# Kernel tuning notes

Hardware: AMD Instinct MI355X
Metric: run time of the kernel (lower is better)

## Reference

```python
import jax, jax.numpy as jnp
import numpy as np

B, T, D = 2, 2048, 2048
H, HD = 8, 128
C = H * HD  # 1024 channels
BT = 64     # chunk size
EPS_RMS = 1.1920929e-07  # torch fp32 finfo eps (RMSNorm default)


def causal_dw_conv(x, w, b):
    # x: [B,T,C], w: [C,4], b: [C]. Equals torch Conv1d(groups=C, k=4, padding=3)[..., :T]
    Bx, Tx, Cx = x.shape
    xp = jnp.pad(x, ((0, 0), (3, 0), (0, 0)))
    out = sum(xp[:, j:j + Tx, :] * w[None, None, :, j] for j in range(4))
    return out + b


def chunk_kda(q, k, v, g):
    # q,k,g: [B,H,T,K]; v: [B,H,T,V]
    Bx, Hx, Tx, K = q.shape
    V = v.shape[-1]
    NT = Tx // BT
    resh = lambda a: a.reshape(Bx, Hx, NT, BT, a.shape[-1])
    q, k, v, g = map(resh, (q, k, v, g))
    gc = jnp.cumsum(g, axis=-2)                        # [B,H,NT,BT,K]
    diff = gc[..., :, None, :] - gc[..., None, :, :]   # [B,H,NT,BT,BT,K]
    tri_incl = jnp.tril(jnp.ones((BT, BT), bool))
    tri_strict = jnp.tril(jnp.ones((BT, BT), bool), -1)
    Aqk = jnp.einsum('bhnik,bhnjk,bhnijk->bhnij', q, k, jnp.exp(diff)) * tri_incl
    Akk = jnp.einsum('bhnik,bhnjk,bhnijk->bhnij', k, k, jnp.exp(-diff)) * tri_strict
    # UT transform: the in-place forward substitution in the source computes
    # A = (I + strictly_lower(Akk))^{-1}; apply it via a unit-lower triangular solve.
    M = Akk + jnp.eye(BT, dtype=q.dtype)
    rhs = jnp.concatenate([jnp.exp(gc) * k, v], axis=-1)
    sol = jax.scipy.linalg.solve_triangular(M, rhs, lower=True, unit_diagonal=True)
    w_, u = sol[..., :K], sol[..., K:]                 # w = A@(exp(gc)*k), u = A@v
    qg = q * jnp.exp(gc)

    def step(S, xs):
        qg_i, k_i, u_i, gc_i, w_i, Aqk_i = xs
        o_i = qg_i @ S + Aqk_i @ (u_i - w_i @ S)
        g_last = gc_i[:, :, -1]                        # [B,H,K]
        decay = jnp.exp(g_last[:, :, None, :] - gc_i)  # [B,H,BT,K]
        S = S * jnp.exp(g_last)[..., :, None] + jnp.einsum('bhck,bhcv->bhkv', k_i * decay, u_i)
        return S, o_i

    xs = tuple(jnp.moveaxis(a, 2, 0) for a in (qg, k, u, gc, w_, Aqk))
    S0 = jnp.zeros((Bx, Hx, K, V), q.dtype)
    S, o = jax.lax.scan(step, S0, xs)
    o = jnp.moveaxis(o, 0, 2).reshape(Bx, Hx, Tx, V)
    return o, S


def _forward(x, Wq, Wk, Wv, conv_q_w, conv_q_b, conv_k_w, conv_k_b, conv_v_w, conv_v_b,
             Wad, Wau, Wb, Wgd, Wgu, norm_w, Wo):
    Bx, Tx, Dx = x.shape
    heads = lambda y: y.reshape(Bx, Tx, H, HD).transpose(0, 2, 1, 3)
    q = heads(causal_dw_conv(x @ Wq, conv_q_w, conv_q_b))
    k = heads(causal_dw_conv(x @ Wk, conv_k_w, conv_k_b))
    q = q / jnp.maximum(jnp.linalg.norm(q, axis=-1, keepdims=True), 1e-12)
    k = k / jnp.maximum(jnp.linalg.norm(k, axis=-1, keepdims=True), 1e-12)
    v = heads(jax.nn.silu(causal_dw_conv(x @ Wv, conv_v_w, conv_v_b)))
    alpha = jax.nn.sigmoid(heads(x @ Wad @ Wau))
    g = jnp.log(jnp.clip(alpha, 1e-6, None))
    _beta = jax.nn.sigmoid(x @ Wb)  # computed in source but unused by chunk_kda
    o, S = chunk_kda(q, k, v, g)
    o = o.transpose(0, 2, 1, 3)                        # [B,T,H,HD]
    o = o * jax.lax.rsqrt(jnp.mean(o * o, axis=-1, keepdims=True) + EPS_RMS) * norm_w
    gate = jax.nn.sigmoid(x @ Wgd @ Wgu).reshape(Bx, Tx, H, HD)
    o = (o * gate).reshape(Bx, Tx, H * HD)
    return o @ Wo, S


def setup_inputs():
    key = jax.random.key(0)
    ks = jax.random.split(key, 16)
    n = lambda k, shape, s=0.02: jax.random.normal(k, shape, jnp.float32) * s
    return {
        'x': jax.random.normal(ks[0], (B, T, D), jnp.float32),
        'Wq': n(ks[1], (D, C)), 'Wk': n(ks[2], (D, C)), 'Wv': n(ks[3], (D, C)),
        'conv_q_w': n(ks[4], (C, 4), 0.1), 'conv_q_b': jnp.zeros((C,), jnp.float32),
        'conv_k_w': n(ks[5], (C, 4), 0.1), 'conv_k_b': jnp.zeros((C,), jnp.float32),
        'conv_v_w': n(ks[6], (C, 4), 0.1), 'conv_v_b': jnp.zeros((C,), jnp.float32),
        'Wad': n(ks[7], (D, HD)), 'Wau': n(ks[8], (HD, C)),
        'Wb': n(ks[9], (D, H)),
        'Wgd': n(ks[10], (D, HD)), 'Wgu': n(ks[11], (HD, C)),
        'norm_w': jnp.ones((HD,), jnp.float32),
        'Wo': n(ks[12], (C, D)),
    }


def reference(x, Wq, Wk, Wv, conv_q_w, conv_q_b, conv_k_w, conv_k_b, conv_v_w, conv_v_b,
              Wad, Wau, Wb, Wgd, Wgu, norm_w, Wo):
    return _forward(x, Wq, Wk, Wv, conv_q_w, conv_q_b, conv_k_w, conv_k_b, conv_v_w, conv_v_b,
                    Wad, Wau, Wb, Wgd, Wgu, norm_w, Wo)
```

## Files before the change

kernel.cpp:

```cpp
#include <hip/hip_runtime.h>
#include <hip/hip_bf16.h>
#include <cstdint>
#include <cstddef>

constexpr int B_  = 2;
constexpr int T_  = 2048;
constexpr int D_  = 2048;
constexpr int H_  = 8;
constexpr int HD_ = 128;
constexpr int C_  = 1024;
constexpr int BT_ = 64;
constexpr int NT_ = 32;
constexpr int M_  = 4096;
constexpr float EPS_RMS = 1.1920929e-07f;

typedef __bf16 bf16x8 __attribute__((ext_vector_type(8)));
typedef float f32x4 __attribute__((ext_vector_type(4)));

typedef const __attribute__((address_space(1))) unsigned int* gptr_t;
typedef __attribute__((address_space(3))) unsigned int* lptr_t;

__device__ __forceinline__ void gload16(const void* g, void* l) {
  __builtin_amdgcn_global_load_lds((gptr_t)g, (lptr_t)l, 16, 0, 0);
}


#define LD_A(base, mq, dst) do { \
    _Pragma("unroll") for (int i_ = 0; i_ < 4; ++i_) \
      _Pragma("unroll") for (int k_ = 0; k_ < 2; ++k_) \
        dst[i_][k_] = *(const bf16x8*)((base) + (mq) * 8192 + i_ * 2048 + k_ * 1024); \
  } while (0)

#define LD_B(base, nq, dst) do { \
    _Pragma("unroll") for (int j_ = 0; j_ < 2; ++j_) \
      _Pragma("unroll") for (int k_ = 0; k_ < 2; ++k_) \
        dst[j_][k_] = *(const bf16x8*)((base) + (nq) * 4096 + j_ * 2048 + k_ * 1024); \
  } while (0)

#define MM_Q(afr, bfr, mq, nq) do { \
    _Pragma("unroll") for (int i_ = 0; i_ < 4; ++i_) \
      _Pragma("unroll") for (int j_ = 0; j_ < 2; ++j_) \
        _Pragma("unroll") for (int k_ = 0; k_ < 2; ++k_) \
          acc[(mq) * 4 + i_][(nq) * 2 + j_] = __builtin_amdgcn_mfma_f32_16x16x32_bf16( \
              afr[i_][k_], bfr[j_][k_], acc[(mq) * 4 + i_][(nq) * 2 + j_], 0, 0, 0); \
  } while (0)

#define STAGE(src, grow0, kc, loff) do { \
    gload16((src) + (size_t)((grow0) + sr0) * 2048 + (kc) + sc0, smem + (loff) + tid * 16); \
    gload16((src) + (size_t)((grow0) + sr1) * 2048 + (kc) + sc1, smem + (loff) + 8192 + tid * 16); \
  } while (0)

#define PH_SYNC_PRE do { \
    __builtin_amdgcn_s_barrier(); \
    asm volatile("s_waitcnt lgkmcnt(0)" ::: "memory"); \
    __builtin_amdgcn_sched_barrier(0); \
    __builtin_amdgcn_s_setprio(1); \
  } while (0)

#define PH_SYNC_POST do { \
    __builtin_amdgcn_s_setprio(0); \
    __builtin_amdgcn_sched_barrier(0); \
    __builtin_amdgcn_s_barrier(); \
  } while (0)

#define PH_SYNC_POST_VM4 do { \
    __builtin_amdgcn_s_setprio(0); \
    __builtin_amdgcn_sched_barrier(0); \
    asm volatile("s_waitcnt vmcnt(4)" ::: "memory"); \
    __builtin_amdgcn_s_barrier(); \
  } while (0)

#define PH_SYNC_POST_VM0 do { \
    __builtin_amdgcn_s_setprio(0); \
    __builtin_amdgcn_sched_barrier(0); \
    asm volatile("s_waitcnt vmcnt(0)" ::: "memory"); \
    __builtin_amdgcn_s_barrier(); \
  } while (0)

__global__ __launch_bounds__(512, 1) void gemm8p(
    const __hip_bfloat16* __restrict__ A_, const __hip_bfloat16* __restrict__ B_,
    __hip_bfloat16* __restrict__ pre, __hip_bfloat16* __restrict__ adb,
    __hip_bfloat16* __restrict__ gdb) {
  __shared__ alignas(16) char smem[131072];
  const int tid = threadIdx.x, lane = tid & 63;
  const int wid = tid >> 6;
  const int wm = (wid >> 2) * 128, wn = (wid & 3) * 64;
  const int lr = lane & 15, lg = lane >> 4;

  const int bid = blockIdx.x;
  const int swz = (bid & 7) * 26 + (bid >> 3);
  const int mt = swz / 13, nt = swz % 13;
  const int m0 = mt * 256, n0g = nt * 256;

  int ob0 = tid * 16;         ob0 ^= ((ob0 >> 9) & 1) << 5;
  int ob1 = (tid + 512) * 16; ob1 ^= ((ob1 >> 9) & 1) << 5;
  const int sr0 = ((ob0 >> 11) << 4) + ((ob0 >> 6) & 15);
  const int sc0 = ((ob0 >> 10) & 1) * 32 + ((ob0 & 63) >> 1);
  const int sr1 = ((ob1 >> 11) << 4) + ((ob1 >> 6) & 15);
  const int sc1 = ((ob1 >> 10) & 1) * 32 + ((ob1 & 63) >> 1);

  const int foff = lr * 64 + ((lg * 16) ^ ((lr & 8) << 2));
  const int bq = (wn & 64) * 128;
  const char* a0base = smem + (wm >> 7) * 16384 + foff;
  const char* a1base = smem + 65536 + (wm >> 7) * 16384 + foff;
  const char* b0base = smem + 32768 + (wn >> 7) * 16384 + bq + foff;
  const char* b1base = smem + 98304 + (wn >> 7) * 16384 + bq + foff;

  f32x4 acc[8][4];
#pragma unroll
  for (int i = 0; i < 8; ++i)
#pragma unroll
    for (int j = 0; j < 4; ++j) acc[i][j] = (f32x4)(0.f);

  bf16x8 a[4][2], b01[2][2], b23[2][2];

  STAGE(A_, m0,        0, 0);
  STAGE(A_, m0 + 128,  0, 16384);
  STAGE(B_, n0g,       0, 32768);
  STAGE(B_, n0g + 128, 0, 32768 + 16384);
  STAGE(B_, n0g,       64, 98304);
  STAGE(B_, n0g + 128, 64, 98304 + 16384);
  asm volatile("s_waitcnt vmcnt(4)" ::: "memory");
  __builtin_amdgcn_s_barrier();

#pragma unroll 1
  for (int it = 0; it < 15; ++it) {
    const int kA1 = (2 * it + 1) * 64;
    const int kN2 = (2 * it + 2) * 64;
    const int kB3 = (2 * it + 3) * 64;
    LD_A(a0base, 0, a);
    LD_B(b0base, 0, b01);
    STAGE(A_, m0, kA1, 65536);
    PH_SYNC_PRE; MM_Q(a, b01, 0, 0); PH_SYNC_POST;
    LD_B(b0base, 1, b23);
    STAGE(A_, m0 + 128, kA1, 65536 + 16384);
    PH_SYNC_PRE; MM_Q(a, b23, 0, 1); PH_SYNC_POST;
    LD_A(a0base, 1, a);
    STAGE(B_, n0g, kN2, 32768);
    PH_SYNC_PRE; MM_Q(a, b23, 1, 1); PH_SYNC_POST;
    STAGE(B_, n0g + 128, kN2, 32768 + 16384);
    PH_SYNC_PRE; MM_Q(a, b01, 1, 0); PH_SYNC_POST_VM4;
    LD_A(a1base, 0, a);
    LD_B(b1base, 0, b01);
    STAGE(A_, m0, kN2, 0);
    PH_SYNC_PRE; MM_Q(a, b01, 0, 0); PH_SYNC_POST;
    LD_B(b1base, 1, b23);
    STAGE(A_, m0 + 128, kN2, 16384);
    PH_SYNC_PRE; MM_Q(a, b23, 0, 1); PH_SYNC_POST;
    LD_A(a1base, 1, a);
    STAGE(B_, n0g, kB3, 98304);
    PH_SYNC_PRE; MM_Q(a, b23, 1, 1); PH_SYNC_POST;
    STAGE(B_, n0g + 128, kB3, 98304 + 16384);
    PH_SYNC_PRE; MM_Q(a, b01, 1, 0); PH_SYNC_POST_VM4;
  }

  {
    const int kT = 1984;
    LD_A(a0base, 0, a);
    LD_B(b0base, 0, b01);
    STAGE(A_, m0, kT, 65536);
    PH_SYNC_PRE; MM_Q(a, b01, 0, 0); PH_SYNC_POST;
    LD_B(b0base, 1, b23);
    STAGE(A_, m0 + 128, kT, 65536 + 16384);
    PH_SYNC_PRE; MM_Q(a, b23, 0, 1); PH_SYNC_POST;
    LD_A(a0base, 1, a);
    PH_SYNC_PRE; MM_Q(a, b23, 1, 1); PH_SYNC_POST;
    PH_SYNC_PRE; MM_Q(a, b01, 1, 0); PH_SYNC_POST_VM0;
    LD_A(a1base, 0, a);
    LD_B(b1base, 0, b01);
    MM_Q(a, b01, 0, 0);
    LD_B(b1base, 1, b23);
    MM_Q(a, b23, 0, 1);
    LD_A(a1base, 1, a);
    MM_Q(a, b23, 1, 1);
    MM_Q(a, b01, 1, 0);
  }

#pragma unroll
  for (int mf = 0; mf < 8; ++mf) {
    const int row0 = m0 + wm + mf * 16 + lg * 4;
#pragma unroll
    for (int nf = 0; nf < 4; ++nf) {
      const int c = n0g + wn + nf * 16 + lr;
#pragma unroll
      for (int r = 0; r < 4; ++r) {
        const __hip_bfloat16 v = __float2bfloat16(acc[mf][nf][r]);
        const size_t rr = (size_t)(row0 + r);
        if (c < 3072)      pre[rr * 3072 + c] = v;
        else if (c < 3200) adb[rr * 128 + (c - 3072)] = v;
        else               gdb[rr * 128 + (c - 3200)] = v;
      }
    }
  }
}

template <typename OutT>
__global__ __launch_bounds__(256) void gemm_bf16k(
    const __hip_bfloat16* __restrict__ A, const __hip_bfloat16* __restrict__ Bt,
    OutT* __restrict__ C, int N, int K) {
  __shared__ __hip_bfloat16 sA[128 * 32];
  __shared__ __hip_bfloat16 sB[128 * 32];
  const int tid = threadIdx.x;
  const int lane = tid & 63;
  const int m0 = blockIdx.y * 128, n0 = blockIdx.x * 128;
  const int wm = ((tid >> 6) >> 1) * 64, wn = ((tid >> 6) & 1) * 64;
  f32x4 acc[4][4];
#pragma unroll
  for (int i = 0; i < 4; ++i)
#pragma unroll
    for (int j = 0; j < 4; ++j) acc[i][j] = (f32x4)(0.f);
  const int f0 = tid, f1 = tid + 256;
  const int r0 = f0 >> 2, c0 = (f0 & 3) * 8;
  const int r1 = f1 >> 2, c1 = (f1 & 3) * 8;
  const size_t aoff0 = (size_t)(m0 + r0) * K + c0;
  const size_t aoff1 = (size_t)(m0 + r1) * K + c1;
  const size_t boff0 = (size_t)(n0 + r0) * K + c0;
  const size_t boff1 = (size_t)(n0 + r1) * K + c1;
  const int lr = lane & 15, lk = (lane >> 4) * 8;
  for (int k0 = 0; k0 < K; k0 += 32) {
    __syncthreads();
    gload16(A + aoff0 + k0, &sA[f0 * 8]);
    gload16(A + aoff1 + k0, &sA[f1 * 8]);
    gload16(Bt + boff0 + k0, &sB[f0 * 8]);
    gload16(Bt + boff1 + k0, &sB[f1 * 8]);
    __syncthreads();
    bf16x8 af[4], bfr[4];
#pragma unroll
    for (int i = 0; i < 4; ++i)
      af[i] = *(const bf16x8*)&sA[(wm + i * 16 + lr) * 32 + lk];
#pragma unroll
    for (int j = 0; j < 4; ++j)
      bfr[j] = *(const bf16x8*)&sB[(wn + j * 16 + lr) * 32 + lk];
#pragma unroll
    for (int i = 0; i < 4; ++i)
#pragma unroll
      for (int j = 0; j < 4; ++j)
        acc[i][j] = __builtin_amdgcn_mfma_f32_16x16x32_bf16(af[i], bfr[j], acc[i][j], 0, 0, 0);
  }
  const int er = (lane >> 4) * 4, ec = lane & 15;
#pragma unroll
  for (int i = 0; i < 4; ++i) {
#pragma unroll
    for (int j = 0; j < 4; ++j) {
      int row = m0 + wm + i * 16 + er;
      int col = n0 + wn + j * 16 + ec;
#pragma unroll
      for (int r = 0; r < 4; ++r) {
        float v = acc[i][j][r];
        if constexpr (sizeof(OutT) == 2)
          C[(size_t)(row + r) * N + col] = __float2bfloat16(v);
        else
          C[(size_t)(row + r) * N + col] = v;
      }
    }
  }
}

__global__ __launch_bounds__(256) void gemm_augu(
    const __hip_bfloat16* __restrict__ ad, const __hip_bfloat16* __restrict__ gd,
    const __hip_bfloat16* __restrict__ Wau, const __hip_bfloat16* __restrict__ Wgu,
    float* __restrict__ gc, float* __restrict__ glast,
    __hip_bfloat16* __restrict__ gatef) {
  constexpr int N = 1024, K = 128;
  __shared__ alignas(16) char smraw[128 * 132 * 4];
  __hip_bfloat16* sA = (__hip_bfloat16*)smraw;
  __hip_bfloat16* sB = (__hip_bfloat16*)(smraw + 8192);
  float (*scan)[132] = (float(*)[132])smraw;

  const int z = blockIdx.z;
  const __hip_bfloat16* A = z ? gd : ad;
  const __hip_bfloat16* Bt = z ? Wgu : Wau;
  const int tid = threadIdx.x;
  const int lane = tid & 63;
  const int m0 = blockIdx.y * 128, n0 = blockIdx.x * 128;
  const int wm = ((tid >> 6) >> 1) * 64, wn = ((tid >> 6) & 1) * 64;
  f32x4 acc[4][4];
#pragma unroll
  for (int i = 0; i < 4; ++i)
#pragma unroll
    for (int j = 0; j < 4; ++j) acc[i][j] = (f32x4)(0.f);
  const int f0 = tid, f1 = tid + 256;
  const int r0 = f0 >> 2, c0 = (f0 & 3) * 8;
  const int r1 = f1 >> 2, c1 = (f1 & 3) * 8;
  const size_t aoff0 = (size_t)(m0 + r0) * K + c0;
  const size_t aoff1 = (size_t)(m0 + r1) * K + c1;
  const size_t boff0 = (size_t)(n0 + r0) * K + c0;
  const size_t boff1 = (size_t)(n0 + r1) * K + c1;
  const int lr = lane & 15, lk = (lane >> 4) * 8;
#pragma unroll
  for (int k0 = 0; k0 < K; k0 += 32) {
    __syncthreads();
    gload16(A + aoff0 + k0, &sA[f0 * 8]);
    gload16(A + aoff1 + k0, &sA[f1 * 8]);
    gload16(Bt + boff0 + k0, &sB[f0 * 8]);
    gload16(Bt + boff1 + k0, &sB[f1 * 8]);
    __syncthreads();
    bf16x8 af[4], bfr[4];
#pragma unroll
    for (int i = 0; i < 4; ++i)
      af[i] = *(const bf16x8*)&sA[(wm + i * 16 + lr) * 32 + lk];
#pragma unroll
    for (int j = 0; j < 4; ++j)
      bfr[j] = *(const bf16x8*)&sB[(wn + j * 16 + lr) * 32 + lk];
#pragma unroll
    for (int i = 0; i < 4; ++i)
#pragma unroll
      for (int j = 0; j < 4; ++j)
        acc[i][j] = __builtin_amdgcn_mfma_f32_16x16x32_bf16(af[i], bfr[j], acc[i][j], 0, 0, 0);
  }
  const int er = (lane >> 4) * 4, ec = lane & 15;
  if (z == 1) {
#pragma unroll
    for (int i = 0; i < 4; ++i)
#pragma unroll
      for (int j = 0; j < 4; ++j) {
        int row = m0 + wm + i * 16 + er;
        int col = n0 + wn + j * 16 + ec;
#pragma unroll
        for (int r = 0; r < 4; ++r)
          gatef[(size_t)(row + r) * N + col] = __float2bfloat16(acc[i][j][r]);
      }
    return;
  }
  __syncthreads();
#pragma unroll
  for (int i = 0; i < 4; ++i)
#pragma unroll
    for (int j = 0; j < 4; ++j) {
      int rowL = wm + i * 16 + er;
      int colL = wn + j * 16 + ec;
#pragma unroll
      for (int r = 0; r < 4; ++r) {
        float a = acc[i][j][r];
        float s = fmaxf(1.f / (1.f + __expf(-a)), 1e-6f);
        scan[rowL + r][colL] = __logf(s);
      }
    }
  __syncthreads();
  {
    const int d = tid & 127, c2 = tid >> 7;
    const int h = blockIdx.x;
    const int b = m0 >> 11, tb = m0 & 2047;
    const int bh = b * H_ + h;
    float run = 0.f;
    const size_t gbase = ((size_t)bh * T_ + tb + c2 * 64) * 128 + d;
    for (int r = 0; r < 64; ++r) {
      run += scan[c2 * 64 + r][d];
      gc[gbase + (size_t)r * 128] = run;
    }
    glast[((size_t)(bh * NT_ + (tb >> 6) + c2)) * 128 + d] = run;
  }
}

__global__ __launch_bounds__(256) void prep(
    const float* __restrict__ x, const float* __restrict__ Wq,
    const float* __restrict__ Wk, const float* __restrict__ Wv,
    const float* __restrict__ Wad, const float* __restrict__ Wgd,
    const float* __restrict__ Wau, const float* __restrict__ Wgu,
    const float* __restrict__ Wo, __hip_bfloat16* __restrict__ xb,
    __hip_bfloat16* __restrict__ Wt_qkv, __hip_bfloat16* __restrict__ Wt_dg,
    __hip_bfloat16* __restrict__ Wt_aug, __hip_bfloat16* __restrict__ Wt_o) {
  __shared__ float tile[32][33];
  int bid = blockIdx.x;
  const int tid = threadIdx.x;
  if (bid < 8192) {
    size_t i = ((size_t)bid * 256 + tid) * 4;
    float4 v = *(const float4*)(x + i);
    xb[i + 0] = __float2bfloat16(v.x);
    xb[i + 1] = __float2bfloat16(v.y);
    xb[i + 2] = __float2bfloat16(v.z);
    xb[i + 3] = __float2bfloat16(v.w);
    return;
  }
  bid -= 8192;
  const float* W; __hip_bfloat16* dst; int K, N, bx, by;
  if (bid < 6144) {
    int z = bid / 2048, r = bid % 2048;
    W = (z == 0) ? Wq : (z == 1) ? Wk : Wv;
    dst = Wt_qkv + (size_t)z * C_ * D_;
    K = D_; N = C_; bx = r & 31; by = r >> 5;
  } else if (bid < 6144 + 512) {
    int b2 = bid - 6144;
    int z = b2 >> 8, r = b2 & 255;
    W = z ? Wgd : Wad;
    dst = Wt_dg + (size_t)z * HD_ * D_;
    K = D_; N = HD_; bx = r & 3; by = r >> 2;
  } else if (bid < 6144 + 512 + 256) {
    int b2 = bid - 6144 - 512;
    int z = b2 >> 7, r = b2 & 127;
    W = z ? Wgu : Wau;
    dst = Wt_aug + (size_t)z * C_ * HD_;
    K = HD_; N = C_; bx = r & 31; by = r >> 5;
  } else {
    int b2 = bid - 6144 - 512 - 256;
    W = Wo; dst = Wt_o;
    K = C_; N = D_; bx = b2 & 63; by = b2 >> 6;
  }
  int tx = tid & 31, ty = tid >> 5;
  int kb = by * 32, nb = bx * 32;
#pragma unroll
  for (int s = 0; s < 4; ++s) {
    int kk = ty + s * 8;
    tile[kk][tx] = W[(size_t)(kb + kk) * N + nb + tx];
  }
  __syncthreads();
#pragma unroll
  for (int s = 0; s < 4; ++s) {
    int nn = ty + s * 8;
    dst[(size_t)(nb + nn) * K + kb + tx] = __float2bfloat16(tile[tx][nn]);
  }
}

__global__ __launch_bounds__(128) void conv_qkv(
    const __hip_bfloat16* __restrict__ pre, const float* __restrict__ gc,
    const float* __restrict__ cqw, const float* __restrict__ cqb,
    const float* __restrict__ ckw, const float* __restrict__ ckb,
    const float* __restrict__ cvw, const float* __restrict__ cvb,
    __hip_bfloat16* __restrict__ qg, __hip_bfloat16* __restrict__ kp,
    __hip_bfloat16* __restrict__ km, __hip_bfloat16* __restrict__ vb) {
  int idx = blockIdx.x;
  int h = idx & 7;
  int t = (idx >> 3) & (T_ - 1);
  int b = idx >> 14;
  int d = threadIdx.x;
  int c = h * HD_ + d;
  const __hip_bfloat16* p = pre + (size_t)(b * T_ + t) * (3 * C_) + c;
  float aq, ak, av;
  {
    float w0 = cqw[c * 4], w1 = cqw[c * 4 + 1], w2 = cqw[c * 4 + 2], w3 = cqw[c * 4 + 3];
    aq = cqb[c] + w3 * __bfloat162float(p[0]);
    if (t > 0) aq += w2 * __bfloat162float(p[-(ptrdiff_t)(3 * C_)]);
    if (t > 1) aq += w1 * __bfloat162float(p[-2 * (ptrdiff_t)(3 * C_)]);
    if (t > 2) aq += w0 * __bfloat162float(p[-3 * (ptrdiff_t)(3 * C_)]);
  }
  {
    const __hip_bfloat16* pk = p + C_;
    float w0 = ckw[c * 4], w1 = ckw[c * 4 + 1], w2 = ckw[c * 4 + 2], w3 = ckw[c * 4 + 3];
    ak = ckb[c] + w3 * __bfloat162float(pk[0]);
    if (t > 0) ak += w2 * __bfloat162float(pk[-(ptrdiff_t)(3 * C_)]);
    if (t > 1) ak += w1 * __bfloat162float(pk[-2 * (ptrdiff_t)(3 * C_)]);
    if (t > 2) ak += w0 * __bfloat162float(pk[-3 * (ptrdiff_t)(3 * C_)]);
  }
  {
    const __hip_bfloat16* pv = p + 2 * C_;
    float w0 = cvw[c * 4], w1 = cvw[c * 4 + 1], w2 = cvw[c * 4 + 2], w3 = cvw[c * 4 + 3];
    av = cvb[c] + w3 * __bfloat162float(pv[0]);
    if (t > 0) av += w2 * __bfloat162float(pv[-(ptrdiff_t)(3 * C_)]);
    if (t > 1) av += w1 * __bfloat162float(pv[-2 * (ptrdiff_t)(3 * C_)]);
    if (t > 2) av += w0 * __bfloat162float(pv[-3 * (ptrdiff_t)(3 * C_)]);
  }
  float ssq = aq * aq, ssk = ak * ak;
#pragma unroll
  for (int o = 1; o < 64; o <<= 1) {
    ssq += __shfl_xor(ssq, o);
    ssk += __shfl_xor(ssk, o);
  }
  __shared__ float red[2][2];
  if ((d & 63) == 0) { red[0][d >> 6] = ssq; red[1][d >> 6] = ssk; }
  __syncthreads();
  float nq = fmaxf(sqrtf(red[0][0] + red[0][1]), 1e-12f);
  float nk = fmaxf(sqrtf(red[1][0] + red[1][1]), 1e-12f);
  size_t oi = (((size_t)b * H_ + h) * T_ + t) * HD_ + d;
  float g = gc[oi];
  float eg = __expf(g), emg = __expf(-g);
  qg[oi] = __float2bfloat16(aq / nq * eg);
  float kn = ak / nk;
  kp[oi] = __float2bfloat16(kn * eg);
  km[oi] = __float2bfloat16(kn * emg);
  vb[oi] = __float2bfloat16(av * (1.f / (1.f + __expf(-av))));
}

__global__ __launch_bounds__(256) void chunk_mid(
    const __hip_bfloat16* __restrict__ qg, const __hip_bfloat16* __restrict__ kp,
    const __hip_bfloat16* __restrict__ km, const __hip_bfloat16* __restrict__ vb,
    __hip_bfloat16* __restrict__ Aq, __hip_bfloat16* __restrict__ w_bf,
    __hip_bfloat16* __restrict__ u_bf, __hip_bfloat16* __restrict__ PT_bf) {
  __shared__ float A_T[64][68];
  __shared__ float solu[64][128];
  __shared__ __hip_bfloat16 kmS[64 * 128];
  const int tid = threadIdx.x;
  const int bhn = blockIdx.x;
  const size_t gbase = ((size_t)(bhn >> 5) * T_ + (size_t)(bhn & 31) * BT_) * HD_;
  const int wv = tid >> 6, lane = tid & 63;
  const int lr = lane & 15, lg = lane >> 4;
  const int prod = wv >> 1, rh = wv & 1;

  {
    const char* src = (const char*)(km + gbase);
#pragma unroll
    for (int s = 0; s < 4; ++s)
      gload16(src + s * 4096 + tid * 16, ((char*)kmS) + s * 4096 + tid * 16);
  }

  {
    const __hip_bfloat16* A = (prod ? qg : km) + gbase;
    const __hip_bfloat16* Bt = (prod ? km : kp) + gbase;
    f32x4 acc[2][4];
#pragma unroll
    for (int i = 0; i < 2; ++i)
#pragma unroll
      for (int j = 0; j < 4; ++j) acc[i][j] = (f32x4)(0.f);
#pragma unroll
    for (int k0 = 0; k0 < 128; k0 += 32) {
      bf16x8 af[2], bfr[4];
#pragma unroll
      for (int i = 0; i < 2; ++i)
        af[i] = *(const bf16x8*)(A + (size_t)(rh * 32 + i * 16 + lr) * 128 + k0 + lg * 8);
#pragma unroll
      for (int j = 0; j < 4; ++j)
        bfr[j] = *(const bf16x8*)(Bt + (size_t)(j * 16 + lr) * 128 + k0 + lg * 8);
#pragma unroll
      for (int i = 0; i < 2; ++i)
#pragma unroll
        for (int j = 0; j < 4; ++j)
          acc[i][j] = __builtin_amdgcn_mfma_f32_16x16x32_bf16(af[i], bfr[j], acc[i][j], 0, 0, 0);
    }
    if (prod == 0) {
#pragma unroll
      for (int i = 0; i < 2; ++i)
#pragma unroll
        for (int j = 0; j < 4; ++j) {
          int row0 = rh * 32 + i * 16 + lg * 4;
          int col = j * 16 + lr;
          *(float4*)&A_T[col][row0] =
              make_float4(acc[i][j][0], acc[i][j][1], acc[i][j][2], acc[i][j][3]);
        }
    } else {
      __hip_bfloat16* dst = Aq + (size_t)bhn * 4096;
#pragma unroll
      for (int i = 0; i < 2; ++i)
#pragma unroll
        for (int j = 0; j < 4; ++j)
#pragma unroll
          for (int r = 0; r < 4; ++r) {
            int row = rh * 32 + i * 16 + lg * 4 + r;
            int col = j * 16 + lr;
            float v = (col <= row) ? acc[i][j][r] : 0.f;
            dst[row * 64 + col] = __float2bfloat16(v);
          }
    }
  }
  __syncthreads();

  {
    const int col = tid & 127;
    const __hip_bfloat16* rhs = ((tid < 128) ? kp : vb) + gbase;
    float s[64];
#pragma unroll
    for (int i = 0; i < 64; ++i)
      s[i] = __bfloat162float(rhs[(size_t)i * 128 + col]);
#pragma unroll
    for (int ib = 0; ib < 64; ib += 4) {
      const float s0 = s[ib];
      const float s1 = fmaf(-A_T[ib][ib + 1], s0, s[ib + 1]);
      const float s2 = fmaf(-A_T[ib + 1][ib + 2], s1,
                       fmaf(-A_T[ib][ib + 2], s0, s[ib + 2]));
      const float s3 = fmaf(-A_T[ib + 2][ib + 3], s2,
                       fmaf(-A_T[ib + 1][ib + 3], s1,
                       fmaf(-A_T[ib][ib + 3], s0, s[ib + 3])));
      s[ib + 1] = s1; s[ib + 2] = s2; s[ib + 3] = s3;
#pragma unroll
      for (int j4 = ib + 4; j4 < 64; j4 += 4) {
        float4 a0 = *(const float4*)&A_T[ib][j4];
        float4 a1 = *(const float4*)&A_T[ib + 1][j4];
        float4 a2 = *(const float4*)&A_T[ib + 2][j4];
        float4 a3 = *(const float4*)&A_T[ib + 3][j4];
        s[j4]     = fmaf(-a3.x, s3, fmaf(-a2.x, s2, fmaf(-a1.x, s1, fmaf(-a0.x, s0, s[j4]))));
        s[j4 + 1] = fmaf(-a3.y, s3, fmaf(-a2.y, s2, fmaf(-a1.y, s1, fmaf(-a0.y, s0, s[j4 + 1]))));
        s[j4 + 2] = fmaf(-a3.z, s3, fmaf(-a2.z, s2, fmaf(-a1.z, s1, fmaf(-a0.z, s0, s[j4 + 2]))));
        s[j4 + 3] = fmaf(-a3.w, s3, fmaf(-a2.w, s2, fmaf(-a1.w, s1, fmaf(-a0.w, s0, s[j4 + 3]))));
      }
    }
    if (tid < 128) {
#pragma unroll
      for (int i = 0; i < 64; ++i)
        w_bf[gbase + (size_t)i * 128 + col] = __float2bfloat16(s[i]);
    } else {
#pragma unroll
      for (int i = 0; i < 64; ++i) {
        u_bf[gbase + (size_t)i * 128 + col] = __float2bfloat16(s[i]);
        solu[i][col] = s[i];
      }
    }
  }
  __syncthreads();

  {
    const int kd0 = (tid & 15) * 8, vd0 = (tid >> 4) * 8;
    float acc[8][8];
#pragma unroll
    for (int a = 0; a < 8; ++a)
#pragma unroll
      for (int b2 = 0; b2 < 8; ++b2) acc[a][b2] = 0.f;
#pragma unroll 4
    for (int i = 0; i < 64; ++i) {
      uint4 rawv = *(const uint4*)&kmS[i * 128 + kd0];
      const __hip_bfloat16* hp = (const __hip_bfloat16*)&rawv;
      float kv[8];
#pragma unroll
      for (int e = 0; e < 8; ++e) kv[e] = __bfloat162float(hp[e]);
      float uv[8];
      *(float4*)(uv)     = *(const float4*)&solu[i][vd0];
      *(float4*)(uv + 4) = *(const float4*)&solu[i][vd0 + 4];
#pragma unroll
      for (int a = 0; a < 8; ++a)
#pragma unroll
        for (int b2 = 0; b2 < 8; ++b2) acc[a][b2] = fmaf(kv[a], uv[b2], acc[a][b2]);
    }
    __hip_bfloat16* dst = PT_bf + (size_t)bhn * 16384;
#pragma unroll
    for (int b2 = 0; b2 < 8; ++b2) {
      union { __hip_bfloat16 hx[8]; uint4 u4; } pk2;
#pragma unroll
      for (int a = 0; a < 8; ++a) pk2.hx[a] = __float2bfloat16(acc[a][b2]);
      *(uint4*)(dst + (size_t)(vd0 + b2) * 128 + kd0) = pk2.u4;
    }
  }
}

__global__ __launch_bounds__(128) void scan_pt(
    const __hip_bfloat16* __restrict__ PT_bf, const float* __restrict__ glast,
    __hip_bfloat16* __restrict__ STg, float* __restrict__ Sout) {
  int vd = blockIdx.x & 127;
  int bh = blockIdx.x >> 7;
  int kd = threadIdx.x;
  float s = 0.f;
  for (int n = 0; n < NT_; ++n) {
    size_t idx = (((size_t)bh * NT_ + n) * HD_ + vd) * HD_ + kd;
    float p = __bfloat162float(PT_bf[idx]);
    STg[idx] = __float2bfloat16(s);
    float gl = glast[((size_t)bh * NT_ + n) * 128 + kd];
    s = (s + p) * __expf(gl);
  }
  Sout[((size_t)bh * HD_ + kd) * HD_ + vd] = s;
}

__global__ __launch_bounds__(256) void chunk_tail(
    const __hip_bfloat16* __restrict__ qg_bf, const __hip_bfloat16* __restrict__ w_bf,
    const __hip_bfloat16* __restrict__ u_bf, const __hip_bfloat16* __restrict__ Aq_bf,
    const __hip_bfloat16* __restrict__ STg, const __hip_bfloat16* __restrict__ gatef,
    const float* __restrict__ normw, __hip_bfloat16* __restrict__ o2b) {
  constexpr int XTS = 72;
  __shared__ __hip_bfloat16 XT[128 * XTS];
  __shared__ float red[64][4];
  __shared__ __hip_bfloat16 uS[64 * 128];
  const int tid = threadIdx.x;
  const int bhn = blockIdx.x;
  const int bh = bhn >> 5, n = bhn & 31;
  const int b = bh >> 3, h = bh & 7;
  const int t0 = n * 64, hoff = h * 128;
  const size_t gbase = ((size_t)bh * T_ + t0) * 128;
  const __hip_bfloat16* Sg = STg + (size_t)bhn * 16384;

  {
    const char* src = (const char*)(u_bf + gbase);
#pragma unroll
    for (int s = 0; s < 4; ++s)
      gload16(src + s * 4096 + tid * 16, ((char*)uS) + s * 4096 + tid * 16);
  }

  const int wv = tid >> 6, lane = tid & 63;
  const int lr = lane & 15, lg = lane >> 4;
  f32x4 accX[4][2], accO[4][2];
#pragma unroll
  for (int i = 0; i < 4; ++i)
#pragma unroll
    for (int j = 0; j < 2; ++j) { accX[i][j] = (f32x4)(0.f); accO[i][j] = (f32x4)(0.f); }

  const __hip_bfloat16* wrow = w_bf + gbase;
  const __hip_bfloat16* qrow = qg_bf + gbase;
#pragma unroll
  for (int k0 = 0; k0 < 128; k0 += 32) {
    bf16x8 aW[4], aQ[4], bS[2];
#pragma unroll
    for (int i = 0; i < 4; ++i) {
      aW[i] = *(const bf16x8*)(wrow + (size_t)(i * 16 + lr) * 128 + k0 + lg * 8);
      aQ[i] = *(const bf16x8*)(qrow + (size_t)(i * 16 + lr) * 128 + k0 + lg * 8);
    }
#pragma unroll
    for (int j = 0; j < 2; ++j)
      bS[j] = *(const bf16x8*)(Sg + (size_t)(wv * 32 + j * 16 + lr) * 128 + k0 + lg * 8);
#pragma unroll
    for (int i = 0; i < 4; ++i)
#pragma unroll
      for (int j = 0; j < 2; ++j) {
        accX[i][j] = __builtin_amdgcn_mfma_f32_16x16x32_bf16(aW[i], bS[j], accX[i][j], 0, 0, 0);
        accO[i][j] = __builtin_amdgcn_mfma_f32_16x16x32_bf16(aQ[i], bS[j], accO[i][j], 0, 0, 0);
      }
  }

  asm volatile("s_waitcnt vmcnt(0)" ::: "memory");
  __builtin_amdgcn_s_barrier();

#pragma unroll
  for (int i = 0; i < 4; ++i)
#pragma unroll
    for (int j = 0; j < 2; ++j) {
      int row0 = i * 16 + lg * 4;
      int col = wv * 32 + j * 16 + lr;
      union { __hip_bfloat16 hx[4]; uint2 u2; } xv;
#pragma unroll
      for (int r = 0; r < 4; ++r) {
        float uu = __bfloat162float(uS[(row0 + r) * 128 + col]);
        xv.hx[r] = __float2bfloat16(uu - accX[i][j][r]);
      }
      *(uint2*)&XT[col * XTS + row0] = xv.u2;
    }
  __syncthreads();

  const __hip_bfloat16* aqb = Aq_bf + (size_t)bhn * 4096;
#pragma unroll
  for (int k0 = 0; k0 < 64; k0 += 32) {
    bf16x8 aA[4], bX[2];
#pragma unroll
    for (int i = 0; i < 4; ++i)
      aA[i] = *(const bf16x8*)(aqb + (size_t)(i * 16 + lr) * 64 + k0 + lg * 8);
#pragma unroll
    for (int j = 0; j < 2; ++j)
      bX[j] = *(const bf16x8*)&XT[(wv * 32 + j * 16 + lr) * XTS + k0 + lg * 8];
#pragma unroll
    for (int i = 0; i < 4; ++i)
#pragma unroll
      for (int j = 0; j < 2; ++j)
        accO[i][j] = __builtin_amdgcn_mfma_f32_16x16x32_bf16(aA[i], bX[j], accO[i][j], 0, 0, 0);
  }

#pragma unroll
  for (int i = 0; i < 4; ++i)
#pragma unroll
    for (int r = 0; r < 4; ++r) {
      int row = i * 16 + lg * 4 + r;
      float o0 = accO[i][0][r], o1 = accO[i][1][r];
      float ss = o0 * o0 + o1 * o1;
#pragma unroll
      for (int o = 1; o < 16; o <<= 1) ss += __shfl_xor(ss, o);
      if (lr == 0) red[row][wv] = ss;
    }
  __syncthreads();
  float nw0 = normw[wv * 32 + lr];
  float nw1 = normw[wv * 32 + 16 + lr];
#pragma unroll
  for (int i = 0; i < 4; ++i)
#pragma unroll
    for (int r = 0; r < 4; ++r) {
      int row = i * 16 + lg * 4 + r;
      float tot = red[row][0] + red[row][1] + red[row][2] + red[row][3];
      float rms = rsqrtf(tot * (1.f / 128.f) + EPS_RMS);
      size_t orow = (size_t)(b * T_ + t0 + row) * C_ + hoff;
      int c0 = wv * 32 + lr, c1 = c0 + 16;
      float g0 = __bfloat162float(gatef[orow + c0]);
      float g1 = __bfloat162float(gatef[orow + c1]);
      float s0 = 1.f / (1.f + __expf(-g0));
      float s1 = 1.f / (1.f + __expf(-g1));
      o2b[orow + c0] = __float2bfloat16(accO[i][0][r] * rms * nw0 * s0);
      o2b[orow + c1] = __float2bfloat16(accO[i][1][r] * rms * nw1 * s1);
    }
}

extern "C" void kernel_launch(void* const* d_in, const int* in_sizes, int n_in,
                              void* d_out, int out_size, void* d_ws, size_t ws_size,
                              hipStream_t stream) {
  (void)in_sizes; (void)n_in; (void)out_size;
  const float* x    = (const float*)d_in[0];
  const float* Wq   = (const float*)d_in[1];
  const float* Wk   = (const float*)d_in[2];
  const float* Wv   = (const float*)d_in[3];
  const float* cqw  = (const float*)d_in[4];
  const float* cqb  = (const float*)d_in[5];
  const float* ckw  = (const float*)d_in[6];
  const float* ckb  = (const float*)d_in[7];
  const float* cvw  = (const float*)d_in[8];
  const float* cvb  = (const float*)d_in[9];
  const float* Wad  = (const float*)d_in[10];
  const float* Wau  = (const float*)d_in[11];
  const float* Wgd  = (const float*)d_in[13];
  const float* Wgu  = (const float*)d_in[14];
  const float* normw= (const float*)d_in[15];
  const float* Wo   = (const float*)d_in[16];

  float* outp = (float*)d_out;
  float* Sout = outp + (size_t)M_ * D_;

  const size_t SZ = (size_t)M_ * C_;

  float* ws = (float*)d_ws;
  __hip_bfloat16* pre_qkv = (__hip_bfloat16*)(ws);
  float* a_full = ws + 3 * SZ / 2;
  __hip_bfloat16* gatef = (__hip_bfloat16*)(ws + 5 * SZ / 2);
  float* gc_g = ws + 3 * SZ;
  __hip_bfloat16* qg_bf = (__hip_bfloat16*)(ws + 4 * SZ);
  __hip_bfloat16* kp_bf = (__hip_bfloat16*)(ws + 9 * SZ / 2);
  __hip_bfloat16* km_bf = (__hip_bfloat16*)(ws + 5 * SZ);
  __hip_bfloat16* v_bf  = (__hip_bfloat16*)(ws + 11 * SZ / 2);
  __hip_bfloat16* w_bf  = (__hip_bfloat16*)(ws + 6 * SZ);
  __hip_bfloat16* u_bf  = (__hip_bfloat16*)(ws + 13 * SZ / 2);
  __hip_bfloat16* Aq_bf = (__hip_bfloat16*)(ws + 7 * SZ);
  float* glast = ws + 29 * SZ / 4;
  __hip_bfloat16* PT_bf = (__hip_bfloat16*)(ws + 15 * SZ / 2);
  __hip_bfloat16* STg   = (__hip_bfloat16*)(ws + 17 * SZ / 2);
  __hip_bfloat16* xb    = (__hip_bfloat16*)(ws + 19 * SZ / 2);
  __hip_bfloat16* Wt_qkv = (__hip_bfloat16*)(ws + 21 * SZ / 2);
  size_t off = 21 * SZ / 2 + 3 * SZ / 4;
  __hip_bfloat16* Wt_dg  = (__hip_bfloat16*)(ws + off); off += 262144;
  __hip_bfloat16* Wt_aug = (__hip_bfloat16*)(ws + off); off += 131072;
  __hip_bfloat16* Wt_o   = (__hip_bfloat16*)(ws + off); off += 1048576;
  __hip_bfloat16* ad_bf  = (__hip_bfloat16*)(ws + off); off += 262144;
  __hip_bfloat16* gd_bf  = (__hip_bfloat16*)(ws + off); off += 262144;
  if (ws_size < off * sizeof(float)) return;

  __hip_bfloat16* o2b = (__hip_bfloat16*)a_full;
  __hip_bfloat16* Wt_au = Wt_aug;
  __hip_bfloat16* Wt_gu = Wt_aug + (size_t)C_ * HD_;

  prep<<<17152, 256, 0, stream>>>(x, Wq, Wk, Wv, Wad, Wgd, Wau, Wgu, Wo,
                                  xb, Wt_qkv, Wt_dg, Wt_aug, Wt_o);

  gemm8p<<<208, 512, 0, stream>>>(xb, Wt_qkv, pre_qkv, ad_bf, gd_bf);
  gemm_augu<<<dim3(C_ / 128, M_ / 128, 2), 256, 0, stream>>>(
      ad_bf, gd_bf, Wt_au, Wt_gu, gc_g, glast, gatef);

  conv_qkv<<<B_ * T_ * H_, 128, 0, stream>>>(pre_qkv, gc_g, cqw, cqb, ckw, ckb,
                                             cvw, cvb, qg_bf, kp_bf, km_bf, v_bf);

  chunk_mid<<<B_ * H_ * NT_, 256, 0, stream>>>(qg_bf, kp_bf, km_bf, v_bf,
                                               Aq_bf, w_bf, u_bf, PT_bf);
  scan_pt<<<B_ * H_ * HD_, 128, 0, stream>>>(PT_bf, glast, STg, Sout);

  chunk_tail<<<B_ * H_ * NT_, 256, 0, stream>>>(qg_bf, w_bf, u_bf, Aq_bf, STg,
                                                gatef, normw, o2b);
  gemm_bf16k<float><<<dim3(D_ / 128, M_ / 128), 256, 0, stream>>>(o2b, Wt_o, outp, D_, C_);
}
```

Baseline: 362.2 us.

## Restructure conv_qkv to per-chunk blocks with sliding window and vectorized IO

```diff
diff --git a/kernel.cpp b/kernel.cpp
--- a/kernel.cpp
+++ b/kernel.cpp
@@ -366,10 +366,12 @@
   if (bid < 8192) {
     size_t i = ((size_t)bid * 256 + tid) * 4;
     float4 v = *(const float4*)(x + i);
-    xb[i + 0] = __float2bfloat16(v.x);
-    xb[i + 1] = __float2bfloat16(v.y);
-    xb[i + 2] = __float2bfloat16(v.z);
-    xb[i + 3] = __float2bfloat16(v.w);
+    union { __hip_bfloat16 hx[4]; uint2 u2; } pk_;
+    pk_.hx[0] = __float2bfloat16(v.x);
+    pk_.hx[1] = __float2bfloat16(v.y);
+    pk_.hx[2] = __float2bfloat16(v.z);
+    pk_.hx[3] = __float2bfloat16(v.w);
+    *(uint2*)(xb + i) = pk_.u2;
     return;
   }
   bid -= 8192;
@@ -411,63 +413,116 @@
   }
 }
 
-__global__ __launch_bounds__(128) void conv_qkv(
+__global__ __launch_bounds__(256) void conv_qkv(
     const __hip_bfloat16* __restrict__ pre, const float* __restrict__ gc,
     const float* __restrict__ cqw, const float* __restrict__ cqb,
     const float* __restrict__ ckw, const float* __restrict__ ckb,
     const float* __restrict__ cvw, const float* __restrict__ cvb,
     __hip_bfloat16* __restrict__ qg, __hip_bfloat16* __restrict__ kp,
     __hip_bfloat16* __restrict__ km, __hip_bfloat16* __restrict__ vb) {
-  int idx = blockIdx.x;
-  int h = idx & 7;
-  int t = (idx >> 3) & (T_ - 1);
-  int b = idx >> 14;
-  int d = threadIdx.x;
-  int c = h * HD_ + d;
-  const __hip_bfloat16* p = pre + (size_t)(b * T_ + t) * (3 * C_) + c;
-  float aq, ak, av;
-  {
-    float w0 = cqw[c * 4], w1 = cqw[c * 4 + 1], w2 = cqw[c * 4 + 2], w3 = cqw[c * 4 + 3];
-    aq = cqb[c] + w3 * __bfloat162float(p[0]);
-    if (t > 0) aq += w2 * __bfloat162float(p[-(ptrdiff_t)(3 * C_)]);
-    if (t > 1) aq += w1 * __bfloat162float(p[-2 * (ptrdiff_t)(3 * C_)]);
-    if (t > 2) aq += w0 * __bfloat162float(p[-3 * (ptrdiff_t)(3 * C_)]);
-  }
-  {
-    const __hip_bfloat16* pk = p + C_;
-    float w0 = ckw[c * 4], w1 = ckw[c * 4 + 1], w2 = ckw[c * 4 + 2], w3 = ckw[c * 4 + 3];
-    ak = ckb[c] + w3 * __bfloat162float(pk[0]);
-    if (t > 0) ak += w2 * __bfloat162float(pk[-(ptrdiff_t)(3 * C_)]);
-    if (t > 1) ak += w1 * __bfloat162float(pk[-2 * (ptrdiff_t)(3 * C_)]);
-    if (t > 2) ak += w0 * __bfloat162float(pk[-3 * (ptrdiff_t)(3 * C_)]);
-  }
-  {
-    const __hip_bfloat16* pv = p + 2 * C_;
-    float w0 = cvw[c * 4], w1 = cvw[c * 4 + 1], w2 = cvw[c * 4 + 2], w3 = cvw[c * 4 + 3];
-    av = cvb[c] + w3 * __bfloat162float(pv[0]);
-    if (t > 0) av += w2 * __bfloat162float(pv[-(ptrdiff_t)(3 * C_)]);
-    if (t > 1) av += w1 * __bfloat162float(pv[-2 * (ptrdiff_t)(3 * C_)]);
-    if (t > 2) av += w0 * __bfloat162float(pv[-3 * (ptrdiff_t)(3 * C_)]);
-  }
-  float ssq = aq * aq, ssk = ak * ak;
-#pragma unroll
-  for (int o = 1; o < 64; o <<= 1) {
-    ssq += __shfl_xor(ssq, o);
-    ssk += __shfl_xor(ssk, o);
-  }
-  __shared__ float red[2][2];
-  if ((d & 63) == 0) { red[0][d >> 6] = ssq; red[1][d >> 6] = ssk; }
-  __syncthreads();
-  float nq = fmaxf(sqrtf(red[0][0] + red[0][1]), 1e-12f);
-  float nk = fmaxf(sqrtf(red[1][0] + red[1][1]), 1e-12f);
-  size_t oi = (((size_t)b * H_ + h) * T_ + t) * HD_ + d;
-  float g = gc[oi];
-  float eg = __expf(g), emg = __expf(-g);
-  qg[oi] = __float2bfloat16(aq / nq * eg);
-  float kn = ak / nk;
-  kp[oi] = __float2bfloat16(kn * eg);
-  km[oi] = __float2bfloat16(kn * emg);
-  vb[oi] = __float2bfloat16(av * (1.f / (1.f + __expf(-av))));
+  const int bhn = blockIdx.x;
+  const int b = bhn >> 8, h = (bhn >> 5) & 7, n = bhn & 31;
+  const int wv = threadIdx.x >> 6, lane = threadIdx.x & 63;
+  const int d0 = lane * 2;
+  const int c0 = h * HD_ + d0;
+
+  float qw[2][4], kw[2][4], vw[2][4], qb2[2], kb2[2], vb2[2];
+#pragma unroll
+  for (int e = 0; e < 2; ++e) {
+    const int c = c0 + e;
+#pragma unroll
+    for (int j = 0; j < 4; ++j) {
+      qw[e][j] = cqw[c * 4 + j];
+      kw[e][j] = ckw[c * 4 + j];
+      vw[e][j] = cvw[c * 4 + j];
+    }
+    qb2[e] = cqb[c]; kb2[e] = ckb[c]; vb2[e] = cvb[c];
+  }
+
+  const int tw0 = n * 64 + wv * 16;
+  const size_t prow0 = ((size_t)b * T_ + tw0) * (3 * C_) + c0;
+
+  float xm[3][3][2];
+#pragma unroll
+  for (int a = 0; a < 3; ++a)
+#pragma unroll
+    for (int g2 = 0; g2 < 3; ++g2) { xm[a][g2][0] = 0.f; xm[a][g2][1] = 0.f; }
+#pragma unroll
+  for (int g2 = 1; g2 <= 3; ++g2) {
+    if (tw0 - g2 >= 0) {
+      const __hip_bfloat16* pr = pre + (prow0 - (size_t)g2 * (3 * C_));
+#pragma unroll
+      for (int a = 0; a < 3; ++a) {
+        uint u = *(const uint*)(pr + a * C_);
+        xm[a][g2 - 1][0] = __bfloat162float(((const __hip_bfloat16*)&u)[0]);
+        xm[a][g2 - 1][1] = __bfloat162float(((const __hip_bfloat16*)&u)[1]);
+      }
+    }
+  }
+
+#pragma unroll
+  for (int i = 0; i < 16; ++i) {
+    const int t = tw0 + i;
+    const __hip_bfloat16* pr = pre + (prow0 + (size_t)i * (3 * C_));
+    float x0[3][2];
+#pragma unroll
+    for (int a = 0; a < 3; ++a) {
+      uint u = *(const uint*)(pr + a * C_);
+      x0[a][0] = __bfloat162float(((const __hip_bfloat16*)&u)[0]);
+      x0[a][1] = __bfloat162float(((const __hip_bfloat16*)&u)[1]);
+    }
+    float aq[2], ak[2], av[2];
+#pragma unroll
+    for (int e = 0; e < 2; ++e) {
+      aq[e] = qb2[e] + qw[e][3] * x0[0][e];
+      if (t > 0) aq[e] += qw[e][2] * xm[0][0][e];
+      if (t > 1) aq[e] += qw[e][1] * xm[0][1][e];
+      if (t > 2) aq[e] += qw[e][0] * xm[0][2][e];
+      ak[e] = kb2[e] + kw[e][3] * x0[1][e];
+      if (t > 0) ak[e] += kw[e][2] * xm[1][0][e];
+      if (t > 1) ak[e] += kw[e][1] * xm[1][1][e];
+      if (t > 2) ak[e] += kw[e][0] * xm[1][2][e];
+      av[e] = vb2[e] + vw[e][3] * x0[2][e];
+      if (t > 0) av[e] += vw[e][2] * xm[2][0][e];
+      if (t > 1) av[e] += vw[e][1] * xm[2][1][e];
+      if (t > 2) av[e] += vw[e][0] * xm[2][2][e];
+    }
+#pragma unroll
+    for (int a = 0; a < 3; ++a) {
+#pragma unroll
+      for (int e = 0; e < 2; ++e) {
+        xm[a][2][e] = xm[a][1][e];
+        xm[a][1][e] = xm[a][0][e];
+        xm[a][0][e] = x0[a][e];
+      }
+    }
+    float ssq = aq[0] * aq[0] + aq[1] * aq[1];
+    float ssk = ak[0] * ak[0] + ak[1] * ak[1];
+#pragma unroll
+    for (int o = 1; o < 64; o <<= 1) {
+      ssq += __shfl_xor(ssq, o);
+      ssk += __shfl_xor(ssk, o);
+    }
+    const float nq = fmaxf(sqrtf(ssq), 1e-12f);
+    const float nk = fmaxf(sqrtf(ssk), 1e-12f);
+    const size_t oi = (((size_t)b * H_ + h) * T_ + t) * HD_ + d0;
+    const float2 gv = *(const float2*)(gc + oi);
+    union { __hip_bfloat16 hx[2]; uint u; } oq, okp, okm, ov;
+#pragma unroll
+    for (int e = 0; e < 2; ++e) {
+      const float g = (e == 0) ? gv.x : gv.y;
+      const float eg = __expf(g), emg = __expf(-g);
+      oq.hx[e]  = __float2bfloat16(aq[e] / nq * eg);
+      const float kn = ak[e] / nk;
+      okp.hx[e] = __float2bfloat16(kn * eg);
+      okm.hx[e] = __float2bfloat16(kn * emg);
+      ov.hx[e]  = __float2bfloat16(av[e] * (1.f / (1.f + __expf(-av[e]))));
+    }
+    *(uint*)(qg + oi) = oq.u;
+    *(uint*)(kp + oi) = okp.u;
+    *(uint*)(km + oi) = okm.u;
+    *(uint*)(vb + oi) = ov.u;
+  }
 }
 
 __global__ __launch_bounds__(256) void chunk_mid(
@@ -819,8 +874,8 @@
   gemm_augu<<<dim3(C_ / 128, M_ / 128, 2), 256, 0, stream>>>(
       ad_bf, gd_bf, Wt_au, Wt_gu, gc_g, glast, gatef);
 
-  conv_qkv<<<B_ * T_ * H_, 128, 0, stream>>>(pre_qkv, gc_g, cqw, cqb, ckw, ckb,
-                                             cvw, cvb, qg_bf, kp_bf, km_bf, v_bf);
+  conv_qkv<<<B_ * H_ * NT_, 256, 0, stream>>>(pre_qkv, gc_g, cqw, cqb, ckw, ckb,
+                                              cvw, cvb, qg_bf, kp_bf, km_bf, v_bf);
 
   chunk_mid<<<B_ * H_ * NT_, 256, 0, stream>>>(qg_bf, kp_bf, km_bf, v_bf,
                                                Aq_bf, w_bf, u_bf, PT_bf);
```

After: 338.2 us. 1.07x faster.
